# Kernel tuning notes

Hardware: AMD Instinct MI355X
Metric: run time of the kernel (lower is better)

Reference implementation:

```python
import jax, jax.numpy as jnp
import numpy as np

N = 100000   # nodes
E = 1600000  # edges (avg degree 16)
G = 128      # graphs in batch
D_IN, D_HID, D_OUT = 128, 256, 128


def setup_inputs() -> dict:
    key = jax.random.key(0)
    ks = jax.random.split(key, 12)
    x = jax.random.normal(ks[0], (N, D_IN), jnp.float32)
    edge_index = jax.random.randint(ks[1], (2, E), 0, N, dtype=jnp.int64)
    batch = jnp.sort(jax.random.randint(ks[2], (N,), 0, G, dtype=jnp.int64))

    def lin(k, i, o):
        return jax.random.normal(k, (i, o), jnp.float32) / np.float32(np.sqrt(i))

    return {
        "x": x, "edge_index": edge_index, "batch": batch,
        "W0": lin(ks[3], D_IN, D_HID),  "b0": jnp.zeros((D_HID,), jnp.float32),
        "W1": lin(ks[4], D_HID, D_HID), "b1": jnp.zeros((D_HID,), jnp.float32),
        "W2": lin(ks[5], D_HID, D_OUT), "b2": jnp.zeros((D_OUT,), jnp.float32),
        "Wf1": lin(ks[6], D_OUT, D_HID), "bf1": jnp.zeros((D_HID,), jnp.float32),
        "Wf2": lin(ks[7], D_HID, 1),     "bf2": jnp.zeros((1,), jnp.float32),
    }


def reference(x, edge_index, batch, W0, b0, W1, b1, W2, b2, Wf1, bf1, Wf2, bf2):
    n = x.shape[0]
    # GCNConv: add self-loops, symmetric deg^{-1/2} normalization,
    # linear transform, scatter-add aggregation, bias added after aggregation
    # (matches PyG GCNConv defaults; dropout is identity in eval mode).
    loop = jnp.arange(n, dtype=edge_index.dtype)
    src = jnp.concatenate([edge_index[0], loop])
    dst = jnp.concatenate([edge_index[1], loop])
    deg = jax.ops.segment_sum(jnp.ones_like(dst, x.dtype), dst, num_segments=n)
    dinv = jax.lax.rsqrt(jnp.maximum(deg, 1.0))  # deg >= 1 after self-loops
    norm = dinv[src] * dinv[dst]                 # [E+N]

    def conv(h, W, b):
        h = h @ W                                # [N, out]
        msg = h[src] * norm[:, None]             # gather + normalize
        return jax.ops.segment_sum(msg, dst, num_segments=n) + b

    h = jax.nn.relu(conv(x, W0, b0))
    h = jax.nn.relu(conv(h, W1, b1))
    h = conv(h, W2, b2)                          # last conv, no relu

    # global mean pool over graphs
    s = jax.ops.segment_sum(h, batch, num_segments=G)
    cnt = jax.ops.segment_sum(jnp.ones((n,), h.dtype), batch, num_segments=G)
    g = s / jnp.maximum(cnt, 1.0)[:, None]       # [G, D_OUT]

    out = jax.nn.relu(g @ Wf1 + bf1)
    return jax.nn.sigmoid(out @ Wf2 + bf2)       # [G, 1]
```

## Files before the change

kernel.cpp:

```cpp
#include <hip/hip_runtime.h>
#include <hip/hip_bf16.h>

typedef __hip_bfloat16 hbf16;
typedef __attribute__((ext_vector_type(8))) short short8;
typedef __attribute__((ext_vector_type(4))) float f32x4;
typedef __attribute__((ext_vector_type(2))) float f32x2;
typedef __attribute__((ext_vector_type(4))) float f32x4v;

static __device__ __forceinline__ float bits2f(unsigned short u) {
  return __uint_as_float(((unsigned)u) << 16);
}
static __device__ __forceinline__ unsigned short f2bits(float f) {
  hbf16 h = __float2bfloat16(f);
  return *reinterpret_cast<unsigned short*>(&h);
}


#define BSH2 9
#define CHUNK 8192

__global__ __launch_bounds__(256) void k_bcnt(
    const int* __restrict__ dst, int e, int nbuk,
    int* __restrict__ bcnt, int* __restrict__ blockOff) {
  __shared__ int hist[1024];
  int t = threadIdx.x;
  int e0 = blockIdx.x * CHUNK;
  int e1 = min(e, e0 + CHUNK);
  for (int b = t; b < nbuk; b += 256) hist[b] = 0;
  __syncthreads();
  for (int i = e0 + t; i < e1; i += 256)
    atomicAdd(&hist[__builtin_nontemporal_load(&dst[i]) >> BSH2], 1);
  __syncthreads();
  for (int b = t; b < nbuk; b += 256) {
    int h = hist[b];
    blockOff[(size_t)blockIdx.x * nbuk + b] = h ? atomicAdd(&bcnt[b], h) : 0;
  }
}

__global__ __launch_bounds__(1024) void k_scanB(
    const int* __restrict__ bcnt, int nbuk, int e,
    int* __restrict__ bstart, int* __restrict__ rowStart, int n) {
  __shared__ int s[1024];
  int t = threadIdx.x;
  int v = (t < nbuk) ? bcnt[t] : 0;
  s[t] = v;
  __syncthreads();
  for (int off = 1; off < 1024; off <<= 1) {
    int x = (t >= off) ? s[t - off] : 0;
    __syncthreads();
    s[t] += x;
    __syncthreads();
  }
  if (t < nbuk) bstart[t] = s[t] - v;
  if (t == 0) { bstart[nbuk] = e; rowStart[n] = e; }
}

__global__ __launch_bounds__(256) void k_partA(
    const int* __restrict__ src, const int* __restrict__ dst, int e, int nbuk,
    const int* __restrict__ bstart, const int* __restrict__ blockOff,
    unsigned* __restrict__ staging) {
  __shared__ int pos[1024];
  int t = threadIdx.x;
  int e0 = blockIdx.x * CHUNK;
  int e1 = min(e, e0 + CHUNK);
  for (int b = t; b < nbuk; b += 256)
    pos[b] = bstart[b] + blockOff[(size_t)blockIdx.x * nbuk + b];
  __syncthreads();
  for (int i = e0 + t; i < e1; i += 256) {
    int d = __builtin_nontemporal_load(&dst[i]);
    int sv = __builtin_nontemporal_load(&src[i]);
    int b = d >> BSH2;
    int r = atomicAdd(&pos[b], 1);
    staging[r] = (unsigned)sv | ((unsigned)(d & 511) << 23);
  }
}

__global__ __launch_bounds__(512) void k_bucket_csr(
    const unsigned* __restrict__ staging, const int* __restrict__ bstart,
    int* __restrict__ rowStart, float* __restrict__ dinv, int* __restrict__ csr, int N) {
  __shared__ int hist[512];
  __shared__ int s[512];
  __shared__ int cnt[512];
  int b = blockIdx.x, t = threadIdx.x;
  int es = bstart[b], ee = bstart[b + 1];
  hist[t] = 0;
  __syncthreads();
  for (int i = es + t; i < ee; i += 512)
    atomicAdd(&hist[staging[i] >> 23], 1);
  __syncthreads();
  s[t] = hist[t];
  __syncthreads();
  for (int off = 1; off < 512; off <<= 1) {
    int x = (t >= off) ? s[t - off] : 0;
    __syncthreads();
    s[t] += x;
    __syncthreads();
  }
  int gpos = es + s[t] - hist[t];
  cnt[t] = gpos;
  int d = (b << BSH2) + t;
  if (d < N) {
    rowStart[d] = gpos;
    dinv[d] = rsqrtf((float)(hist[t] + 1));
  }
  __syncthreads();
  for (int i = es + t; i < ee; i += 512) {
    unsigned w = staging[i];
    int pos = atomicAdd(&cnt[w >> 23], 1);
    csr[pos] = (int)(w & 0x7fffffu);
  }
}

__global__ void k_wt_all(const float* __restrict__ W0, const float* __restrict__ W1,
                         const float* __restrict__ W2, unsigned short* __restrict__ W0t,
                         unsigned short* __restrict__ W1t, unsigned short* __restrict__ W2t) {
  int i = blockIdx.x * blockDim.x + threadIdx.x;
  const float* W; unsigned short* Wt; int K, M, idx;
  if (i < 32768)       { W = W0; Wt = W0t; K = 128; M = 256; idx = i; }
  else if (i < 98304)  { W = W1; Wt = W1t; K = 256; M = 256; idx = i - 32768; }
  else if (i < 131072) { W = W2; Wt = W2t; K = 256; M = 128; idx = i - 98304; }
  else return;
  int m = idx / K, k = idx - m * K;
  Wt[idx] = f2bits(W[k * M + m]);
}

__global__ void k_cast_fp8(const float* __restrict__ x, const float* __restrict__ dinv,
                           unsigned* __restrict__ y, int n4) {
  int i = blockIdx.x * blockDim.x + threadIdx.x;
  if (i < n4) {
    float s = 16.f * dinv[i >> 5];
    f32x4v v = __builtin_nontemporal_load(reinterpret_cast<const f32x4v*>(x) + i);
    unsigned q = 0;
    q = __builtin_amdgcn_cvt_pk_fp8_f32(v[0] * s, v[1] * s, q, false);
    q = __builtin_amdgcn_cvt_pk_fp8_f32(v[2] * s, v[3] * s, q, true);
    y[i] = q;
  }
}


template<int VPL>
static __device__ __forceinline__ unsigned agg8_load(
    const void* __restrict__ h8, int idx, int lane) {
  if constexpr (VPL == 4)
    return reinterpret_cast<const unsigned*>(h8)[(size_t)idx * 64 + lane];
  else
    return (unsigned)reinterpret_cast<const unsigned short*>(h8)[(size_t)idx * 64 + lane];
}

template<int VPL>
static __device__ __forceinline__ void agg8_add(unsigned v, float* acc) {
  f32x2 lo = __builtin_amdgcn_cvt_pk_f32_fp8(v, false);
  acc[0] += lo[0]; acc[1] += lo[1];
  if constexpr (VPL == 4) {
    f32x2 hi = __builtin_amdgcn_cvt_pk_f32_fp8(v, true);
    acc[2] += hi[0]; acc[3] += hi[1];
  }
}

template<int VPL, int U>
static __device__ __forceinline__ void agg8_chunk(
    const void* __restrict__ h8, const int* __restrict__ csr,
    int k, int lane, float* acc) {
  unsigned v[U];
#pragma unroll
  for (int u = 0; u < U; ++u) {
    int idx = __builtin_nontemporal_load(&csr[k + u]);
    v[u] = agg8_load<VPL>(h8, idx, lane);
  }
#pragma unroll
  for (int u = 0; u < U; ++u) agg8_add<VPL>(v[u], acc);
}

template<int D, int BIAS>
__global__ __launch_bounds__(256) void aggregate_f8(
    const void* __restrict__ h8, const int* __restrict__ csr,
    const int* __restrict__ rowStart, const float* __restrict__ dinv,
    const float* __restrict__ bias, void* __restrict__ outv, int N) {
  constexpr int VPL = D / 64;
  int lane = threadIdx.x & 63;
  int d = (blockIdx.x * 256 + threadIdx.x) >> 6;
  if (d >= N) return;
  int rs = __builtin_amdgcn_readfirstlane(rowStart[d]);
  int re = __builtin_amdgcn_readfirstlane(rowStart[d + 1]);

  float acc[VPL] = {};
  agg8_add<VPL>(agg8_load<VPL>(h8, d, lane), acc);

  int k = rs;
  for (; k + 16 <= re; k += 16) agg8_chunk<VPL, 16>(h8, csr, k, lane, acc);
  if (k + 8 <= re) { agg8_chunk<VPL, 8>(h8, csr, k, lane, acc); k += 8; }
  if (k + 4 <= re) { agg8_chunk<VPL, 4>(h8, csr, k, lane, acc); k += 4; }
  for (; k < re; ++k) {
    int idx = __builtin_nontemporal_load(&csr[k]);
    agg8_add<VPL>(agg8_load<VPL>(h8, idx, lane), acc);
  }

  float dv = dinv[d];
  float v[VPL];
#pragma unroll
  for (int j = 0; j < VPL; ++j) {
    v[j] = acc[j] * dv;
    if (BIAS) v[j] += 16.f * bias[lane * VPL + j];
  }
  if constexpr (VPL == 4) {
    unsigned q = 0;
    q = __builtin_amdgcn_cvt_pk_fp8_f32(v[0], v[1], q, false);
    q = __builtin_amdgcn_cvt_pk_fp8_f32(v[2], v[3], q, true);
    reinterpret_cast<unsigned*>(outv)[(size_t)d * 64 + lane] = q;
  } else {
    unsigned q = __builtin_amdgcn_cvt_pk_fp8_f32(v[0], v[1], 0, false);
    reinterpret_cast<unsigned short*>(outv)[(size_t)d * 64 + lane] = (unsigned short)q;
  }
}


#define GLD16(g, l) __builtin_amdgcn_global_load_lds(                         \
    (const __attribute__((address_space(1))) void*)(g),                       \
    (__attribute__((address_space(3))) void*)(l), 16, 0, 0)

static __device__ __forceinline__ void dq_store(uint4 v, char* lA, int r, int c8) {
  unsigned ow[8];
#pragma unroll
  for (int j = 0; j < 4; ++j) {
    unsigned w = (&v.x)[j];
    f32x2 lo = __builtin_amdgcn_cvt_pk_f32_fp8(w, false);
    f32x2 hi = __builtin_amdgcn_cvt_pk_f32_fp8(w, true);
    ow[2 * j]     = (unsigned)f2bits(lo[0]) | ((unsigned)f2bits(lo[1]) << 16);
    ow[2 * j + 1] = (unsigned)f2bits(hi[0]) | ((unsigned)f2bits(hi[1]) << 16);
  }
  int s0 = (c8 * 2) ^ (r & 7);
  int s1 = (c8 * 2 + 1) ^ (r & 7);
  *reinterpret_cast<uint4*>(lA + r * 128 + s0 * 16) = make_uint4(ow[0], ow[1], ow[2], ow[3]);
  *reinterpret_cast<uint4*>(lA + r * 128 + s1 * 16) = make_uint4(ow[4], ow[5], ow[6], ow[7]);
}

template<int K, int EPI>
__global__ __launch_bounds__(256) void gemm_mfma(
    const unsigned char* __restrict__ A8, const unsigned short* __restrict__ Bt,
    const float* __restrict__ bias, const float* __restrict__ dinv,
    unsigned char* __restrict__ C8, int N, int M) {
  __shared__ __align__(16) char smem[32768];
  char* lA = smem;
  char* lB = smem + 16384;
  int tid = threadIdx.x, lane = tid & 63, wid = tid >> 6;
  int rowBase = blockIdx.x * 128, colBase = blockIdx.y * 128;
  int wr = (wid >> 1) * 64, wc = (wid & 1) * 64;

  f32x4 zero = {0.f, 0.f, 0.f, 0.f};
  f32x4 acc[4][4];
#pragma unroll
  for (int m = 0; m < 4; ++m)
#pragma unroll
    for (int n = 0; n < 4; ++n) acc[m][n] = zero;

  const char* Bb = (const char*)Bt;
  int ar = tid >> 1, ah = tid & 1;
  int ga = min(rowBase + ar, N - 1);

  for (int k0 = 0; k0 < K; k0 += 64) {
#pragma unroll
    for (int r = 0; r < 4; ++r) {
      int pbase = r * 256 + wid * 64;
      int p = pbase + lane;
      int row = p >> 3;
      int offg = ((p & 7) * 16) ^ ((row & 7) << 4);
      int gb = colBase + row;
      GLD16(Bb + (size_t)gb * (K * 2) + k0 * 2 + offg, lB + pbase * 16);
    }
    {
      const unsigned char* Ap = A8 + (size_t)ga * K + k0 + ah * 32;
      uint4 va = *reinterpret_cast<const uint4*>(Ap);
      uint4 vb = *reinterpret_cast<const uint4*>(Ap + 16);
      dq_store(va, lA, ar, ah * 2);
      dq_store(vb, lA, ar, ah * 2 + 1);
    }
    __syncthreads();
    int l15 = lane & 15, lhi = lane >> 4;
#pragma unroll
    for (int kk = 0; kk < 2; ++kk) {
      short8 af[4], bfr[4];
      int koff = kk * 64 + lhi * 16;
#pragma unroll
      for (int m = 0; m < 4; ++m) {
        int row = wr + m * 16 + l15;
        af[m] = *reinterpret_cast<const short8*>(lA + row * 128 + (koff ^ ((row & 7) << 4)));
      }
#pragma unroll
      for (int n = 0; n < 4; ++n) {
        int col = wc + n * 16 + l15;
        bfr[n] = *reinterpret_cast<const short8*>(lB + col * 128 + (koff ^ ((col & 7) << 4)));
      }
#pragma unroll
      for (int m = 0; m < 4; ++m)
#pragma unroll
        for (int n = 0; n < 4; ++n)
          acc[m][n] = __builtin_amdgcn_mfma_f32_16x16x32_bf16(af[m], bfr[n], acc[m][n], 0, 0, 0);
    }
    __syncthreads();
  }

  int l15 = lane & 15, lhi = lane >> 4;
  float dvv[4][4];
  if (EPI == 2 || EPI == 3) {
#pragma unroll
    for (int m = 0; m < 4; ++m)
#pragma unroll
      for (int r = 0; r < 4; ++r) {
        int row = rowBase + wr + m * 16 + lhi * 4 + r;
        float dq = (row < N) ? dinv[row] : 1.f;
        dvv[m][r] = (EPI == 2) ? 16.f * dq : dq;
      }
  }
#pragma unroll
  for (int n = 0; n < 4; ++n) {
    int col = colBase + wc + n * 16 + l15;
    float bv = (EPI == 2 || EPI == 4) ? bias[col] : 0.f;
#pragma unroll
    for (int m = 0; m < 4; ++m) {
#pragma unroll
      for (int r = 0; r < 4; ++r) {
        int row = rowBase + wr + m * 16 + lhi * 4 + r;
        if (row < N) {
          float a16 = acc[m][n][r];
          float v;
          if (EPI == 2) {
            v = fmaxf(fmaf(a16, 0.0625f, bv), 0.f) * dvv[m][r];
          } else if (EPI == 3) {
            v = a16 * dvv[m][r];
          } else {
            v = fmaxf(a16 + 16.f * bv, 0.f);
          }
          unsigned pk = __builtin_amdgcn_cvt_pk_fp8_f32(v, v, 0, false);
          C8[(size_t)row * M + col] = (unsigned char)pk;
        }
      }
    }
  }
}


__global__ void graph_bounds(const int* batch, int n, int g_cnt, int* gstart) {
  int g = blockIdx.x * blockDim.x + threadIdx.x;
  if (g > g_cnt) return;
  int lo = 0, hi = n;
  while (lo < hi) {
    int mid = (lo + hi) >> 1;
    if (batch[mid] < g) lo = mid + 1; else hi = mid;
  }
  gstart[g] = lo;
}

__global__ void pool_partial(const unsigned char* __restrict__ h8,
                             const int* __restrict__ batch, int N, float* gbuf) {
  int per = (N + gridDim.x - 1) / gridDim.x;
  int lo = blockIdx.x * per;
  int hi = min(N, lo + per);
  if (lo >= hi) return;
  int t = threadIdx.x;
  int cur = batch[lo];
  float acc = 0.f;
  for (int i = lo; i < hi; ++i) {
    int g = batch[i];
    if (g != cur) {
      atomicAdd(&gbuf[cur * 128 + t], acc);
      acc = 0.f;
      cur = g;
    }
    unsigned b = (unsigned)__builtin_nontemporal_load(&h8[(size_t)i * 128 + t]);
    f32x2 lo2 = __builtin_amdgcn_cvt_pk_f32_fp8(b, false);
    acc += lo2[0];
  }
  atomicAdd(&gbuf[cur * 128 + t], acc);
}


__global__ __launch_bounds__(256) void mlp(const float* __restrict__ gbuf,
                                           const int* __restrict__ gstart,
                                           const float* __restrict__ Wf1,
                                           const float* __restrict__ bf1,
                                           const float* __restrict__ Wf2,
                                           const float* __restrict__ bf2,
                                           float* __restrict__ out) {
  __shared__ float gs[128];
  __shared__ float hid[256];
  int b = blockIdx.x, t = threadIdx.x;
  float inv = 0.0625f / (float)max(gstart[b + 1] - gstart[b], 1);
  if (t < 128) gs[t] = gbuf[b * 128 + t] * inv;
  __syncthreads();
  float acc = bf1[t];
  for (int k = 0; k < 128; ++k) acc += gs[k] * Wf1[k * 256 + t];
  acc = fmaxf(acc, 0.f);
  hid[t] = acc * Wf2[t];
  __syncthreads();
  for (int s2 = 128; s2 > 0; s2 >>= 1) {
    if (t < s2) hid[t] += hid[t + s2];
    __syncthreads();
  }
  if (t == 0) out[b] = 1.f / (1.f + expf(-(hid[0] + bf2[0])));
}


extern "C" void kernel_launch(void* const* d_in, const int* in_sizes, int n_in,
                              void* d_out, int out_size, void* d_ws, size_t ws_size,
                              hipStream_t stream) {
  const float* x   = (const float*)d_in[0];
  const int* ei    = (const int*)d_in[1];
  const int* batch = (const int*)d_in[2];
  const float* W0  = (const float*)d_in[3];
  const float* b0  = (const float*)d_in[4];
  const float* W1  = (const float*)d_in[5];
  const float* b1  = (const float*)d_in[6];
  const float* W2  = (const float*)d_in[7];
  const float* b2  = (const float*)d_in[8];
  const float* Wf1 = (const float*)d_in[9];
  const float* bf1 = (const float*)d_in[10];
  const float* Wf2 = (const float*)d_in[11];
  const float* bf2 = (const float*)d_in[12];
  float* out = (float*)d_out;

  const int DIN = 128, DH = 256, DOUT = 128, G = 128;
  const int N = in_sizes[0] / DIN;
  const int E = in_sizes[1] / 2;
  const int* src = ei;
  const int* dst = ei + E;
  const int NBUK = (N + 511) >> BSH2;
  const int NCHUNK = (E + CHUNK - 1) / CHUNK;

  char* p = (char*)d_ws;
  auto alloc = [&](size_t bytes) {
    char* r = p;
    p += (bytes + 255) & ~(size_t)255;
    return r;
  };
  int* bcnt     = (int*)alloc((size_t)NBUK * 4);
  int* blockOff = (int*)alloc((size_t)NCHUNK * NBUK * 4);
  int* bstart   = (int*)alloc((size_t)(NBUK + 1) * 4);
  int* rowStart = (int*)alloc((size_t)(N + 1) * 4);
  float* dinv   = (float*)alloc((size_t)N * 4);
  int* csr      = (int*)alloc((size_t)E * 4);
  int* gstart   = (int*)alloc((size_t)(G + 1) * 4);
  float* gbuf   = (float*)alloc((size_t)G * DOUT * 4);
  unsigned short* W0t = (unsigned short*)alloc((size_t)DIN * DH * 2);
  unsigned short* W1t = (unsigned short*)alloc((size_t)DH * DH * 2);
  unsigned short* W2t = (unsigned short*)alloc((size_t)DH * DOUT * 2);
  char* S1 = (char*)alloc((size_t)N * DH * 2);
  char* S2 = (char*)alloc((size_t)N * DH * 2);

  unsigned* staging = (unsigned*)S2;

  unsigned*      xb8     = (unsigned*)S1;
  unsigned char* agg0_8  = (unsigned char*)S2;
  unsigned char* h1s8    = (unsigned char*)S1;
  unsigned char* agg1_8  = (unsigned char*)S2;
  unsigned char* h2_8    = (unsigned char*)S1;
  unsigned char* t2s8    = (unsigned char*)S2;
  unsigned char* aggout8 = (unsigned char*)S1;

  const int tb = 256;
  hipMemsetAsync(bcnt, 0, (size_t)NBUK * 4, stream);
  hipMemsetAsync(gbuf, 0, (size_t)G * DOUT * 4, stream);

  k_bcnt<<<NCHUNK, 256, 0, stream>>>(dst, E, NBUK, bcnt, blockOff);
  k_scanB<<<1, 1024, 0, stream>>>(bcnt, NBUK, E, bstart, rowStart, N);
  k_partA<<<NCHUNK, 256, 0, stream>>>(src, dst, E, NBUK, bstart, blockOff, staging);
  k_bucket_csr<<<NBUK, 512, 0, stream>>>(staging, bstart, rowStart, dinv, csr, N);

  k_wt_all<<<(131072 + tb - 1) / tb, tb, 0, stream>>>(W0, W1, W2, W0t, W1t, W2t);

  int n4 = N * DIN / 4;
  k_cast_fp8<<<(n4 + tb - 1) / tb, tb, 0, stream>>>(x, dinv, xb8, n4);

  int gx = (N + 127) / 128;
  int ga = (N + 3) / 4;

  aggregate_f8<128, 0><<<ga, 256, 0, stream>>>(xb8, csr, rowStart, dinv, nullptr, agg0_8, N);
  gemm_mfma<128, 2><<<dim3(gx, 2), 256, 0, stream>>>(agg0_8, W0t, b0, dinv, h1s8, N, DH);

  aggregate_f8<256, 0><<<ga, 256, 0, stream>>>(h1s8, csr, rowStart, dinv, nullptr, agg1_8, N);
  gemm_mfma<256, 4><<<dim3(gx, 2), 256, 0, stream>>>(agg1_8, W1t, b1, nullptr, h2_8, N, DH);

  gemm_mfma<256, 3><<<dim3(gx, 1), 256, 0, stream>>>(h2_8, W2t, nullptr, dinv, t2s8, N, DOUT);
  aggregate_f8<128, 1><<<ga, 256, 0, stream>>>(t2s8, csr, rowStart, dinv, b2, aggout8, N);

  graph_bounds<<<1, 256, 0, stream>>>(batch, N, G, gstart);
  pool_partial<<<1000, 128, 0, stream>>>(aggout8, batch, N, gbuf);
  mlp<<<G, 256, 0, stream>>>(gbuf, gstart, Wf1, bf1, Wf2, bf2, out);
}
```

Measured before the change: 373.6 us.

## Split aggregation feature dimension across two interleaved blocks per node chunk

Each destination node's feature row is now split into two halves, each handled by a separate wavefront in a different block. Blocks are interleaved in groups of eight so the two halves of the same node chunk run close together in time and share cached csr indices. This doubles the number of wavefronts to expose more memory-level parallelism for the gathers. The cost is narrower per-lane loads (bytes instead of words), duplicated reads of csr and rowStart, and twice as many blocks.

```diff
diff --git a/kernel.cpp b/kernel.cpp
--- a/kernel.cpp
+++ b/kernel.cpp
@@ -138,78 +138,115 @@
 }
 
 
-template<int VPL>
-static __device__ __forceinline__ unsigned agg8_load(
-    const void* __restrict__ h8, int idx, int lane) {
-  if constexpr (VPL == 4)
-    return reinterpret_cast<const unsigned*>(h8)[(size_t)idx * 64 + lane];
-  else
-    return (unsigned)reinterpret_cast<const unsigned short*>(h8)[(size_t)idx * 64 + lane];
-}
-
-template<int VPL>
-static __device__ __forceinline__ void agg8_add(unsigned v, float* acc) {
-  f32x2 lo = __builtin_amdgcn_cvt_pk_f32_fp8(v, false);
-  acc[0] += lo[0]; acc[1] += lo[1];
-  if constexpr (VPL == 4) {
-    f32x2 hi = __builtin_amdgcn_cvt_pk_f32_fp8(v, true);
-    acc[2] += hi[0]; acc[3] += hi[1];
-  }
-}
-
-template<int VPL, int U>
-static __device__ __forceinline__ void agg8_chunk(
-    const void* __restrict__ h8, const int* __restrict__ csr,
-    int k, int lane, float* acc) {
-  unsigned v[U];
-#pragma unroll
-  for (int u = 0; u < U; ++u) {
-    int idx = __builtin_nontemporal_load(&csr[k + u]);
-    v[u] = agg8_load<VPL>(h8, idx, lane);
-  }
-#pragma unroll
-  for (int u = 0; u < U; ++u) agg8_add<VPL>(v[u], acc);
-}
-
 template<int D, int BIAS>
-__global__ __launch_bounds__(256) void aggregate_f8(
+__global__ __launch_bounds__(256) void aggregate_f8_s2(
     const void* __restrict__ h8, const int* __restrict__ csr,
     const int* __restrict__ rowStart, const float* __restrict__ dinv,
     const float* __restrict__ bias, void* __restrict__ outv, int N) {
-  constexpr int VPL = D / 64;
+  int bid = blockIdx.x;
+  int r = bid & 7;
+  int s = r >> 2;
+  int chunk = (bid >> 3) * 4 + (r & 3);
   int lane = threadIdx.x & 63;
-  int d = (blockIdx.x * 256 + threadIdx.x) >> 6;
+  int d = chunk * 4 + (threadIdx.x >> 6);
   if (d >= N) return;
   int rs = __builtin_amdgcn_readfirstlane(rowStart[d]);
   int re = __builtin_amdgcn_readfirstlane(rowStart[d + 1]);
-
-  float acc[VPL] = {};
-  agg8_add<VPL>(agg8_load<VPL>(h8, d, lane), acc);
-
-  int k = rs;
-  for (; k + 16 <= re; k += 16) agg8_chunk<VPL, 16>(h8, csr, k, lane, acc);
-  if (k + 8 <= re) { agg8_chunk<VPL, 8>(h8, csr, k, lane, acc); k += 8; }
-  if (k + 4 <= re) { agg8_chunk<VPL, 4>(h8, csr, k, lane, acc); k += 4; }
-  for (; k < re; ++k) {
-    int idx = __builtin_nontemporal_load(&csr[k]);
-    agg8_add<VPL>(agg8_load<VPL>(h8, idx, lane), acc);
-  }
-
-  float dv = dinv[d];
-  float v[VPL];
-#pragma unroll
-  for (int j = 0; j < VPL; ++j) {
-    v[j] = acc[j] * dv;
-    if (BIAS) v[j] += 16.f * bias[lane * VPL + j];
-  }
-  if constexpr (VPL == 4) {
-    unsigned q = 0;
-    q = __builtin_amdgcn_cvt_pk_fp8_f32(v[0], v[1], q, false);
-    q = __builtin_amdgcn_cvt_pk_fp8_f32(v[2], v[3], q, true);
-    reinterpret_cast<unsigned*>(outv)[(size_t)d * 64 + lane] = q;
+  size_t off = (size_t)s * 64 + lane;
+
+  if constexpr (D == 256) {
+    const unsigned short* h16 = (const unsigned short*)h8;
+    float a0 = 0.f, a1 = 0.f;
+    {
+      f32x2 f = __builtin_amdgcn_cvt_pk_f32_fp8((unsigned)h16[(size_t)d * 128 + off], false);
+      a0 += f[0]; a1 += f[1];
+    }
+    int k = rs;
+    for (; k + 16 <= re; k += 16) {
+      unsigned short v[16];
+#pragma unroll
+      for (int u = 0; u < 16; ++u) {
+        int idx = __builtin_nontemporal_load(&csr[k + u]);
+        v[u] = h16[(size_t)idx * 128 + off];
+      }
+#pragma unroll
+      for (int u = 0; u < 16; ++u) {
+        f32x2 f = __builtin_amdgcn_cvt_pk_f32_fp8((unsigned)v[u], false);
+        a0 += f[0]; a1 += f[1];
+      }
+    }
+    if (k + 8 <= re) {
+      unsigned short v[8];
+#pragma unroll
+      for (int u = 0; u < 8; ++u) {
+        int idx = __builtin_nontemporal_load(&csr[k + u]);
+        v[u] = h16[(size_t)idx * 128 + off];
+      }
+#pragma unroll
+      for (int u = 0; u < 8; ++u) {
+        f32x2 f = __builtin_amdgcn_cvt_pk_f32_fp8((unsigned)v[u], false);
+        a0 += f[0]; a1 += f[1];
+      }
+      k += 8;
+    }
+    for (; k < re; ++k) {
+      int idx = __builtin_nontemporal_load(&csr[k]);
+      f32x2 f = __builtin_amdgcn_cvt_pk_f32_fp8((unsigned)h16[(size_t)idx * 128 + off], false);
+      a0 += f[0]; a1 += f[1];
+    }
+    float dv = dinv[d];
+    float v0 = a0 * dv, v1 = a1 * dv;
+    if (BIAS) {
+      v0 += 16.f * bias[s * 128 + lane * 2];
+      v1 += 16.f * bias[s * 128 + lane * 2 + 1];
+    }
+    unsigned q = __builtin_amdgcn_cvt_pk_fp8_f32(v0, v1, 0, false);
+    ((unsigned short*)outv)[(size_t)d * 128 + off] = (unsigned short)q;
   } else {
-    unsigned q = __builtin_amdgcn_cvt_pk_fp8_f32(v[0], v[1], 0, false);
-    reinterpret_cast<unsigned short*>(outv)[(size_t)d * 64 + lane] = (unsigned short)q;
+    const unsigned char* hb = (const unsigned char*)h8;
+    float a0 = 0.f;
+    {
+      f32x2 f = __builtin_amdgcn_cvt_pk_f32_fp8((unsigned)hb[(size_t)d * 128 + off], false);
+      a0 += f[0];
+    }
+    int k = rs;
+    for (; k + 16 <= re; k += 16) {
+      unsigned char v[16];
+#pragma unroll
+      for (int u = 0; u < 16; ++u) {
+        int idx = __builtin_nontemporal_load(&csr[k + u]);
+        v[u] = hb[(size_t)idx * 128 + off];
+      }
+#pragma unroll
+      for (int u = 0; u < 16; ++u) {
+        f32x2 f = __builtin_amdgcn_cvt_pk_f32_fp8((unsigned)v[u], false);
+        a0 += f[0];
+      }
+    }
+    if (k + 8 <= re) {
+      unsigned char v[8];
+#pragma unroll
+      for (int u = 0; u < 8; ++u) {
+        int idx = __builtin_nontemporal_load(&csr[k + u]);
+        v[u] = hb[(size_t)idx * 128 + off];
+      }
+#pragma unroll
+      for (int u = 0; u < 8; ++u) {
+        f32x2 f = __builtin_amdgcn_cvt_pk_f32_fp8((unsigned)v[u], false);
+        a0 += f[0];
+      }
+      k += 8;
+    }
+    for (; k < re; ++k) {
+      int idx = __builtin_nontemporal_load(&csr[k]);
+      f32x2 f = __builtin_amdgcn_cvt_pk_f32_fp8((unsigned)hb[(size_t)idx * 128 + off], false);
+      a0 += f[0];
+    }
+    float dv = dinv[d];
+    float v0 = a0 * dv;
+    if (BIAS) v0 += 16.f * bias[off];
+    unsigned q = __builtin_amdgcn_cvt_pk_fp8_f32(v0, v0, 0, false);
+    ((unsigned char*)outv)[(size_t)d * 128 + off] = (unsigned char)q;
   }
 }
 
@@ -471,16 +508,17 @@
   k_cast_fp8<<<(n4 + tb - 1) / tb, tb, 0, stream>>>(x, dinv, xb8, n4);
 
   int gx = (N + 127) / 128;
-  int ga = (N + 3) / 4;
-
-  aggregate_f8<128, 0><<<ga, 256, 0, stream>>>(xb8, csr, rowStart, dinv, nullptr, agg0_8, N);
+  int C4 = (N + 3) / 4;
+  int Ts = ((2 * C4 + 7) / 8) * 8;
+
+  aggregate_f8_s2<128, 0><<<Ts, 256, 0, stream>>>(xb8, csr, rowStart, dinv, nullptr, agg0_8, N);
   gemm_mfma<128, 2><<<dim3(gx, 2), 256, 0, stream>>>(agg0_8, W0t, b0, dinv, h1s8, N, DH);
 
-  aggregate_f8<256, 0><<<ga, 256, 0, stream>>>(h1s8, csr, rowStart, dinv, nullptr, agg1_8, N);
+  aggregate_f8_s2<256, 0><<<Ts, 256, 0, stream>>>(h1s8, csr, rowStart, dinv, nullptr, agg1_8, N);
   gemm_mfma<256, 4><<<dim3(gx, 2), 256, 0, stream>>>(agg1_8, W1t, b1, nullptr, h2_8, N, DH);
 
   gemm_mfma<256, 3><<<dim3(gx, 1), 256, 0, stream>>>(h2_8, W2t, nullptr, dinv, t2s8, N, DOUT);
-  aggregate_f8<128, 1><<<ga, 256, 0, stream>>>(t2s8, csr, rowStart, dinv, b2, aggout8, N);
+  aggregate_f8_s2<128, 1><<<Ts, 256, 0, stream>>>(t2s8, csr, rowStart, dinv, b2, aggout8, N);
 
   graph_bounds<<<1, 256, 0, stream>>>(batch, N, G, gstart);
   pool_partial<<<1000, 128, 0, stream>>>(aggout8, batch, N, gbuf);
```

New measurement: 502.2 us. +34.4%, slower.
